# Kernel optimization log

Measured on AMD Instinct MI355X. Metric: run time of the kernel, lower is better.

## Reference

```python
import jax, jax.numpy as jnp
import numpy as np

TEMPERATURE = 0.5


def _cos_sim_flat(a, b):
    # row-normalize then full similarity matrix, flattened (matches torch.mm(a_n, b_n.T).flatten())
    a_n = a / jnp.linalg.norm(a, axis=1, keepdims=True)
    b_n = b / jnp.linalg.norm(b, axis=1, keepdims=True)
    return (a_n @ b_n.T).reshape(-1)


def setup_inputs() -> dict:
    key = jax.random.key(0)
    k1, k2, k3 = jax.random.split(key, 3)
    N, D = 4096, 2048
    return {
        "x_source": jax.random.normal(k1, (N, D), dtype=jnp.float32),
        "x_bc_target": jax.random.normal(k2, (N, D), dtype=jnp.float32),
        "x_raw_target": jax.random.normal(k3, (N, D), dtype=jnp.float32),
    }


def reference(x_source, x_bc_target, x_raw_target):
    sim_pos = _cos_sim_flat(x_source, x_bc_target)  # [N*N]
    sim_neg = _cos_sim_flat(x_source, x_raw_target)  # [N*N]
    # denom = sum_j exp(sim_neg_j / T); loss_i = -log(exp(sim_pos_i/T)/denom)
    # = -sim_pos_i/T + logsumexp(sim_neg/T); mean over i. Same math as the
    # original scalar loops, computed as one fused reduction.
    log_denom = jax.nn.logsumexp(sim_neg / TEMPERATURE)
    cl_loss = jnp.mean(log_denom - sim_pos / TEMPERATURE)
    return cl_loss
```

## Files before the change

### kernel.cpp

```cpp
#include <hip/hip_runtime.h>
#include <hip/hip_bf16.h>

#define NR 4096
#define DD 2048
#define INV_T 2.0f
#define QSCALE 32.0f
#define ACC_TO_LOGIT (INV_T / (QSCALE * QSCALE))
#define QS4 64.0f
#define ACC4_TO_LOGIT (INV_T / (QS4 * QS4))

typedef __attribute__((ext_vector_type(2))) float floatx2;
typedef __attribute__((ext_vector_type(4))) float floatx4;
typedef __attribute__((ext_vector_type(4))) int int4v;
typedef __attribute__((ext_vector_type(8))) int int8v;

static __device__ __forceinline__ void async_copy16(const void* g, void* lds) {
  __builtin_amdgcn_global_load_lds((const __attribute__((address_space(1))) void*)g,
                                   (__attribute__((address_space(3))) void*)lds,
                                   16, 0, 0);
}

static __device__ __forceinline__ unsigned int enc4(float x) {
  float u = fminf(fabsf(x), 6.0f);
  int c = (u >= 0.25f) + (u >= 0.75f) + (u >= 1.25f) + (u >= 1.75f) +
          (u >= 2.5f) + (u >= 3.5f) + (u >= 5.0f);
  return (unsigned)(c | (x < 0.f ? 8 : 0));
}

static __device__ __forceinline__ unsigned int pack8_fp4(
    const float4& v0, const float4& v1, float s) {
  return enc4(v0.x * s)        | (enc4(v0.y * s) << 4)  |
         (enc4(v0.z * s) << 8) | (enc4(v0.w * s) << 12) |
         (enc4(v1.x * s) << 16)| (enc4(v1.y * s) << 20) |
         (enc4(v1.z * s) << 24)| (enc4(v1.w * s) << 28);
}

__global__ __launch_bounds__(256) void normalize_kernel(
    const float* __restrict__ src, const float* __restrict__ bc,
    const float* __restrict__ raw,
    unsigned char* __restrict__ a8row, unsigned int* __restrict__ a4,
    unsigned char* __restrict__ b8, unsigned int* __restrict__ c4,
    float* __restrict__ zbuf) {
  const int row = blockIdx.x;
  const int mat = blockIdx.y;
  const int tid = threadIdx.x;
  const float* base = (mat == 0) ? src : ((mat == 1) ? bc : raw);
  const float4* b4 = (const float4*)(base + (size_t)row * DD);

  if (mat == 1 && row < 17) {
    const int idx = row * 256 + tid;
    if (idx < 2 * DD + 1) zbuf[idx] = 0.f;
  }

  float4 v0 = b4[tid * 2];
  float4 v1 = b4[tid * 2 + 1];
  float ss = v0.x * v0.x + v0.y * v0.y + v0.z * v0.z + v0.w * v0.w +
             v1.x * v1.x + v1.y * v1.y + v1.z * v1.z + v1.w * v1.w;
  #pragma unroll
  for (int off = 32; off > 0; off >>= 1) ss += __shfl_down(ss, off, 64);

  __shared__ float sred[4];
  __shared__ float sinv;
  if ((tid & 63) == 0) sred[tid >> 6] = ss;
  __syncthreads();
  if (tid == 0) sinv = rsqrtf(sred[0] + sred[1] + sred[2] + sred[3]);
  __syncthreads();

  if (mat == 2) {
    c4[row * (DD / 8) + tid] = pack8_fp4(v0, v1, sinv * QS4);
    return;
  }

  const float s = sinv * QSCALE;
  int d0 = __builtin_amdgcn_cvt_pk_fp8_f32(v0.x * s, v0.y * s, 0, false);
  d0 = __builtin_amdgcn_cvt_pk_fp8_f32(v0.z * s, v0.w * s, d0, true);
  int d1 = __builtin_amdgcn_cvt_pk_fp8_f32(v1.x * s, v1.y * s, 0, false);
  d1 = __builtin_amdgcn_cvt_pk_fp8_f32(v1.z * s, v1.w * s, d1, true);
  int2 o; o.x = d0; o.y = d1;
  if (mat == 0) {
    *(int2*)(a8row + (size_t)row * DD + tid * 8) = o;
    a4[row * (DD / 8) + tid] = pack8_fp4(v0, v1, sinv * QS4);
  } else {
    *(int2*)(b8 + (size_t)row * DD + tid * 8) = o;
  }
}

__global__ __launch_bounds__(256, 2) void gemm_expsum_kernel(
    const unsigned char* __restrict__ a4, const unsigned char* __restrict__ c4,
    float* __restrict__ S_part) {
  __shared__ unsigned char As[2][128 * 128];
  __shared__ unsigned char Cs[2][128 * 128];
  const int tid = threadIdx.x;
  const int lane = tid & 63;
  const int wave = tid >> 6;
  const int wr = wave >> 1;
  const int wc = wave & 1;
  const int quad = lane >> 4;
  const int l16 = lane & 15;
  const int bc = blockIdx.x, br = blockIdx.y;

  floatx4 acc[4][4] = {};

  const int wrow = lane >> 3;
  const int csrc = (lane & 7) ^ (wrow & 7);
  const unsigned char* gA[4];
  const unsigned char* gC[4];
  int ldsOff[4];
  #pragma unroll
  for (int q = 0; q < 4; q++) {
    const int m = wave * 4 + q;
    const int row = m * 8 + wrow;
    gA[q] = a4 + (size_t)(br * 128 + row) * 1024 + csrc * 16;
    gC[q] = c4 + (size_t)(bc * 128 + row) * 1024 + csrc * 16;
    ldsOff[q] = m * 1024;
  }

  #pragma unroll
  for (int q = 0; q < 4; q++) {
    async_copy16(gA[q], &As[0][ldsOff[q]]);
    async_copy16(gC[q], &Cs[0][ldsOff[q]]);
    gA[q] += 128; gC[q] += 128;
  }

  const int NKT = DD / 256;
  #pragma unroll 2
  for (int kt = 0; kt < NKT; kt++) {
    const int cur = kt & 1;
    __syncthreads();

    if (kt < NKT - 1) {
      #pragma unroll
      for (int q = 0; q < 4; q++) {
        async_copy16(gA[q], &As[cur ^ 1][ldsOff[q]]);
        async_copy16(gC[q], &Cs[cur ^ 1][ldsOff[q]]);
        gA[q] += 128; gC[q] += 128;
      }
    }

    int4v af[2][4], bf[2][4];
    #pragma unroll
    for (int s = 0; s < 2; s++) {
      #pragma unroll
      for (int i = 0; i < 4; i++) {
        const int r = wr * 64 + i * 16 + l16;
        const int pc = (s * 4 + quad) ^ (r & 7);
        af[s][i] = *(const int4v*)&As[cur][r * 128 + pc * 16];
      }
      #pragma unroll
      for (int j = 0; j < 4; j++) {
        const int r = wc * 64 + j * 16 + l16;
        const int pc = (s * 4 + quad) ^ (r & 7);
        bf[s][j] = *(const int4v*)&Cs[cur][r * 128 + pc * 16];
      }
    }
    #pragma unroll
    for (int s = 0; s < 2; s++)
      #pragma unroll
      for (int i = 0; i < 4; i++) {
        const int8v a8v = int8v{af[s][i][0], af[s][i][1], af[s][i][2],
                                af[s][i][3], 0, 0, 0, 0};
        #pragma unroll
        for (int j = 0; j < 4; j++) {
          const int8v b8v = int8v{bf[s][j][0], bf[s][j][1], bf[s][j][2],
                                  bf[s][j][3], 0, 0, 0, 0};
          acc[i][j] = __builtin_amdgcn_mfma_scale_f32_16x16x128_f8f6f4(
              a8v, b8v, acc[i][j], 4 , 4 ,
              0, 0x7F7F7F7F, 0, 0x7F7F7F7F );
        }
      }
  }

  float local = 0.f;
  #pragma unroll
  for (int i = 0; i < 4; i++)
    #pragma unroll
    for (int j = 0; j < 4; j++)
      #pragma unroll
      for (int r = 0; r < 4; r++)
        local += __expf(acc[i][j][r] * ACC4_TO_LOGIT);
  #pragma unroll
  for (int off = 32; off > 0; off >>= 1) local += __shfl_down(local, off, 64);
  __shared__ float red[4];
  if (lane == 0) red[wave] = local;
  __syncthreads();
  if (tid == 0) S_part[br * 32 + bc] = red[0] + red[1] + red[2] + red[3];
}

__global__ __launch_bounds__(256) void colsum_finalize_kernel(
    const unsigned char* __restrict__ a8, const unsigned char* __restrict__ b8,
    float* __restrict__ s_a, float* __restrict__ s_b,
    float* __restrict__ counter, const float* __restrict__ S_part,
    float* __restrict__ out) {
  __shared__ float lds[32 * 264];
  const int tid = threadIdx.x;
  const int rt = tid >> 3;
  const int ct = tid & 7;
  const int cg = blockIdx.x & 7;
  const int rg = blockIdx.x >> 3;
  const int cbase = cg * 256 + ct * 32;
  const int rbase = rg * 256 + rt;

  float accA[32], accB[32];
  #pragma unroll
  for (int i = 0; i < 32; i++) { accA[i] = 0.f; accB[i] = 0.f; }

  #pragma unroll
  for (int k = 0; k < 8; k++) {
    const size_t off = (size_t)(rbase + k * 32) * DD + cbase;
    const int8v ra = *(const int8v*)(a8 + off);
    const int8v rb = *(const int8v*)(b8 + off);
    #pragma unroll
    for (int u = 0; u < 8; u++) {
      floatx2 lo = __builtin_amdgcn_cvt_pk_f32_fp8(ra[u], false);
      floatx2 hi = __builtin_amdgcn_cvt_pk_f32_fp8(ra[u], true);
      accA[u * 4 + 0] += lo[0]; accA[u * 4 + 1] += lo[1];
      accA[u * 4 + 2] += hi[0]; accA[u * 4 + 3] += hi[1];
      lo = __builtin_amdgcn_cvt_pk_f32_fp8(rb[u], false);
      hi = __builtin_amdgcn_cvt_pk_f32_fp8(rb[u], true);
      accB[u * 4 + 0] += lo[0]; accB[u * 4 + 1] += lo[1];
      accB[u * 4 + 2] += hi[0]; accB[u * 4 + 3] += hi[1];
    }
  }

  #pragma unroll
  for (int i = 0; i < 32; i += 4)
    *(floatx4*)&lds[rt * 264 + ct * 32 + i] =
        floatx4{accA[i], accA[i + 1], accA[i + 2], accA[i + 3]};
  __syncthreads();
  float sA = 0.f;
  #pragma unroll 8
  for (int r = 0; r < 32; r++) sA += lds[r * 264 + tid];
  atomicAdd(&s_a[cg * 256 + tid], sA);
  __syncthreads();

  #pragma unroll
  for (int i = 0; i < 32; i += 4)
    *(floatx4*)&lds[rt * 264 + ct * 32 + i] =
        floatx4{accB[i], accB[i + 1], accB[i + 2], accB[i + 3]};
  __syncthreads();
  float sB = 0.f;
  #pragma unroll 8
  for (int r = 0; r < 32; r++) sB += lds[r * 264 + tid];
  atomicAdd(&s_b[cg * 256 + tid], sB);

  __threadfence();
  __syncthreads();
  __shared__ bool amLast;
  if (tid == 0) amLast = (atomicAdd(counter, 1.0f) == 127.0f);
  __syncthreads();
  if (!amLast) return;
  __threadfence();

  float dot = 0.f;
  for (int d = tid; d < DD; d += 256)
    dot += atomicAdd(&s_a[d], 0.f) * atomicAdd(&s_b[d], 0.f);
  float se = 0.f;
  for (int i = tid; i < 1024; i += 256) se += S_part[i];

  #pragma unroll
  for (int off = 32; off > 0; off >>= 1) {
    dot += __shfl_down(dot, off, 64);
    se += __shfl_down(se, off, 64);
  }
  __shared__ float redd[4], reds[4];
  if ((tid & 63) == 0) { redd[tid >> 6] = dot; reds[tid >> 6] = se; }
  __syncthreads();
  if (tid == 0) {
    const float dt = redd[0] + redd[1] + redd[2] + redd[3];
    const float st = reds[0] + reds[1] + reds[2] + reds[3];
    out[0] = logf(st) - dt * (ACC_TO_LOGIT / ((float)NR * (float)NR));
  }
}

extern "C" void kernel_launch(void* const* d_in, const int* in_sizes, int n_in,
                              void* d_out, int out_size, void* d_ws, size_t ws_size,
                              hipStream_t stream) {
  const float* src = (const float*)d_in[0];
  const float* bc  = (const float*)d_in[1];
  const float* raw = (const float*)d_in[2];

  char* ws = (char*)d_ws;
  unsigned char* a8row = (unsigned char*)ws;
  unsigned char* b8 = (unsigned char*)(ws + (size_t)8 * 1024 * 1024);
  unsigned int* a4  = (unsigned int*)(ws + (size_t)16 * 1024 * 1024);
  unsigned int* c4  = (unsigned int*)(ws + (size_t)20 * 1024 * 1024);
  float* zbuf  = (float*)(ws + (size_t)24 * 1024 * 1024);
  float* s_a   = zbuf;
  float* s_b   = zbuf + DD;
  float* counter = zbuf + 2 * DD;
  float* S_part = (float*)(ws + (size_t)24 * 1024 * 1024 + 20480);

  normalize_kernel<<<dim3(NR, 3), 256, 0, stream>>>(src, bc, raw, a8row, a4,
                                                    b8, c4, zbuf);
  gemm_expsum_kernel<<<dim3(32, 32), 256, 0, stream>>>(
      (const unsigned char*)a4, (const unsigned char*)c4, S_part);
  colsum_finalize_kernel<<<128, 256, 0, stream>>>(a8row, b8, s_a, s_b, counter,
                                                  S_part, (float*)d_out);
}
```

Before: 163.9 us.

## Fuse column sums into normalization, drop fp8 copies, remap GEMM tiles per XCD

The normalize kernel now handles 16 rows per block and accumulates the normalized column sums of source and positive-target in fp32 registers. It then reduces them through LDS and adds them atomically into global buffers. This removes the fp8 intermediate matrices and the separate column-sum pass that re-read them. The GEMM block index is remapped so neighbouring tiles land on the same XCD for better L2 reuse. A small zero kernel and a single-block finalize kernel replace the last-block counter logic, which adds launches but makes the positive-term sum more precise.

```diff
diff --git a/kernel.cpp b/kernel.cpp
--- a/kernel.cpp
+++ b/kernel.cpp
@@ -1,11 +1,8 @@
 #include <hip/hip_runtime.h>
-#include <hip/hip_bf16.h>
 
 #define NR 4096
 #define DD 2048
 #define INV_T 2.0f
-#define QSCALE 32.0f
-#define ACC_TO_LOGIT (INV_T / (QSCALE * QSCALE))
 #define QS4 64.0f
 #define ACC4_TO_LOGIT (INV_T / (QS4 * QS4))
 
@@ -35,53 +32,77 @@
          (enc4(v1.z * s) << 24)| (enc4(v1.w * s) << 28);
 }
 
-__global__ __launch_bounds__(256) void normalize_kernel(
+__global__ __launch_bounds__(256) void zero_kernel(floatx4* z) {
+  #pragma unroll
+  for (int i = 0; i < 4; i++)
+    z[threadIdx.x + 256 * i] = floatx4{0.f, 0.f, 0.f, 0.f};
+}
+
+__global__ __launch_bounds__(256) void normalize_colsum_kernel(
     const float* __restrict__ src, const float* __restrict__ bc,
     const float* __restrict__ raw,
-    unsigned char* __restrict__ a8row, unsigned int* __restrict__ a4,
-    unsigned char* __restrict__ b8, unsigned int* __restrict__ c4,
-    float* __restrict__ zbuf) {
-  const int row = blockIdx.x;
+    unsigned int* __restrict__ a4, unsigned int* __restrict__ c4,
+    float* __restrict__ s_a, float* __restrict__ s_b) {
   const int mat = blockIdx.y;
   const int tid = threadIdx.x;
+  const int lane = tid & 63;
+  const int wave = tid >> 6;
   const float* base = (mat == 0) ? src : ((mat == 1) ? bc : raw);
-  const float4* b4 = (const float4*)(base + (size_t)row * DD);
-
-  if (mat == 1 && row < 17) {
-    const int idx = row * 256 + tid;
-    if (idx < 2 * DD + 1) zbuf[idx] = 0.f;
-  }
-
-  float4 v0 = b4[tid * 2];
-  float4 v1 = b4[tid * 2 + 1];
-  float ss = v0.x * v0.x + v0.y * v0.y + v0.z * v0.z + v0.w * v0.w +
-             v1.x * v1.x + v1.y * v1.y + v1.z * v1.z + v1.w * v1.w;
-  #pragma unroll
-  for (int off = 32; off > 0; off >>= 1) ss += __shfl_down(ss, off, 64);
-
-  __shared__ float sred[4];
-  __shared__ float sinv;
-  if ((tid & 63) == 0) sred[tid >> 6] = ss;
+  unsigned int* q4 = (mat == 0) ? a4 : c4;
+
+  float acc[32];
+  #pragma unroll
+  for (int i = 0; i < 32; i++) acc[i] = 0.f;
+
+  #pragma unroll
+  for (int r = 0; r < 4; r++) {
+    const int row = blockIdx.x * 16 + wave * 4 + r;
+    const float4* rp = (const float4*)(base + (size_t)row * DD);
+    float4 v[8];
+    #pragma unroll
+    for (int c = 0; c < 4; c++) {
+      v[2 * c]     = rp[lane * 2 + 128 * c];
+      v[2 * c + 1] = rp[lane * 2 + 1 + 128 * c];
+    }
+    float ss = 0.f;
+    #pragma unroll
+    for (int c = 0; c < 8; c++)
+      ss += v[c].x * v[c].x + v[c].y * v[c].y + v[c].z * v[c].z + v[c].w * v[c].w;
+    #pragma unroll
+    for (int off = 1; off < 64; off <<= 1) ss += __shfl_xor(ss, off, 64);
+    const float sinv = rsqrtf(ss);
+
+    if (mat != 2) {
+      #pragma unroll
+      for (int c = 0; c < 8; c++) {
+        acc[c * 4 + 0] += v[c].x * sinv; acc[c * 4 + 1] += v[c].y * sinv;
+        acc[c * 4 + 2] += v[c].z * sinv; acc[c * 4 + 3] += v[c].w * sinv;
+      }
+    }
+    if (mat != 1) {
+      const float s4 = sinv * QS4;
+      #pragma unroll
+      for (int c = 0; c < 4; c++)
+        q4[row * 256 + lane + 64 * c] = pack8_fp4(v[2 * c], v[2 * c + 1], s4);
+    }
+  }
+  if (mat == 2) return;
+
+  __shared__ float lsum[4][2048];
+  #pragma unroll
+  for (int c = 0; c < 4; c++) {
+    *(floatx4*)&lsum[wave][8 * lane + 512 * c] =
+        floatx4{acc[8 * c], acc[8 * c + 1], acc[8 * c + 2], acc[8 * c + 3]};
+    *(floatx4*)&lsum[wave][8 * lane + 512 * c + 4] =
+        floatx4{acc[8 * c + 4], acc[8 * c + 5], acc[8 * c + 6], acc[8 * c + 7]};
+  }
   __syncthreads();
-  if (tid == 0) sinv = rsqrtf(sred[0] + sred[1] + sred[2] + sred[3]);
-  __syncthreads();
-
-  if (mat == 2) {
-    c4[row * (DD / 8) + tid] = pack8_fp4(v0, v1, sinv * QS4);
-    return;
-  }
-
-  const float s = sinv * QSCALE;
-  int d0 = __builtin_amdgcn_cvt_pk_fp8_f32(v0.x * s, v0.y * s, 0, false);
-  d0 = __builtin_amdgcn_cvt_pk_fp8_f32(v0.z * s, v0.w * s, d0, true);
-  int d1 = __builtin_amdgcn_cvt_pk_fp8_f32(v1.x * s, v1.y * s, 0, false);
-  d1 = __builtin_amdgcn_cvt_pk_fp8_f32(v1.z * s, v1.w * s, d1, true);
-  int2 o; o.x = d0; o.y = d1;
-  if (mat == 0) {
-    *(int2*)(a8row + (size_t)row * DD + tid * 8) = o;
-    a4[row * (DD / 8) + tid] = pack8_fp4(v0, v1, sinv * QS4);
-  } else {
-    *(int2*)(b8 + (size_t)row * DD + tid * 8) = o;
+  float* dst = (mat == 0) ? s_a : s_b;
+  #pragma unroll
+  for (int k = 0; k < 8; k++) {
+    const int col = tid + 256 * k;
+    atomicAdd(&dst[col],
+              lsum[0][col] + lsum[1][col] + lsum[2][col] + lsum[3][col]);
   }
 }
 
@@ -97,7 +118,12 @@
   const int wc = wave & 1;
   const int quad = lane >> 4;
   const int l16 = lane & 15;
-  const int bc = blockIdx.x, br = blockIdx.y;
+
+  const int lin = blockIdx.y * 32 + blockIdx.x;
+  const int xcd = lin & 7;
+  const int idx = lin >> 3;
+  const int br = (xcd >> 1) * 8 + (idx >> 4);
+  const int bc = (xcd & 1) * 16 + (idx & 15);
 
   floatx4 acc[4][4] = {};
 
@@ -186,81 +212,20 @@
   if (tid == 0) S_part[br * 32 + bc] = red[0] + red[1] + red[2] + red[3];
 }
 
-__global__ __launch_bounds__(256) void colsum_finalize_kernel(
-    const unsigned char* __restrict__ a8, const unsigned char* __restrict__ b8,
-    float* __restrict__ s_a, float* __restrict__ s_b,
-    float* __restrict__ counter, const float* __restrict__ S_part,
-    float* __restrict__ out) {
-  __shared__ float lds[32 * 264];
+__global__ __launch_bounds__(256) void finalize_kernel(
+    const float* __restrict__ s_a, const float* __restrict__ s_b,
+    const float* __restrict__ S_part, float* __restrict__ out) {
   const int tid = threadIdx.x;
-  const int rt = tid >> 3;
-  const int ct = tid & 7;
-  const int cg = blockIdx.x & 7;
-  const int rg = blockIdx.x >> 3;
-  const int cbase = cg * 256 + ct * 32;
-  const int rbase = rg * 256 + rt;
-
-  float accA[32], accB[32];
-  #pragma unroll
-  for (int i = 0; i < 32; i++) { accA[i] = 0.f; accB[i] = 0.f; }
-
-  #pragma unroll
-  for (int k = 0; k < 8; k++) {
-    const size_t off = (size_t)(rbase + k * 32) * DD + cbase;
-    const int8v ra = *(const int8v*)(a8 + off);
-    const int8v rb = *(const int8v*)(b8 + off);
-    #pragma unroll
-    for (int u = 0; u < 8; u++) {
-      floatx2 lo = __builtin_amdgcn_cvt_pk_f32_fp8(ra[u], false);
-      floatx2 hi = __builtin_amdgcn_cvt_pk_f32_fp8(ra[u], true);
-      accA[u * 4 + 0] += lo[0]; accA[u * 4 + 1] += lo[1];
-      accA[u * 4 + 2] += hi[0]; accA[u * 4 + 3] += hi[1];
-      lo = __builtin_amdgcn_cvt_pk_f32_fp8(rb[u], false);
-      hi = __builtin_amdgcn_cvt_pk_f32_fp8(rb[u], true);
-      accB[u * 4 + 0] += lo[0]; accB[u * 4 + 1] += lo[1];
-      accB[u * 4 + 2] += hi[0]; accB[u * 4 + 3] += hi[1];
-    }
-  }
-
-  #pragma unroll
-  for (int i = 0; i < 32; i += 4)
-    *(floatx4*)&lds[rt * 264 + ct * 32 + i] =
-        floatx4{accA[i], accA[i + 1], accA[i + 2], accA[i + 3]};
-  __syncthreads();
-  float sA = 0.f;
-  #pragma unroll 8
-  for (int r = 0; r < 32; r++) sA += lds[r * 264 + tid];
-  atomicAdd(&s_a[cg * 256 + tid], sA);
-  __syncthreads();
-
-  #pragma unroll
-  for (int i = 0; i < 32; i += 4)
-    *(floatx4*)&lds[rt * 264 + ct * 32 + i] =
-        floatx4{accB[i], accB[i + 1], accB[i + 2], accB[i + 3]};
-  __syncthreads();
-  float sB = 0.f;
-  #pragma unroll 8
-  for (int r = 0; r < 32; r++) sB += lds[r * 264 + tid];
-  atomicAdd(&s_b[cg * 256 + tid], sB);
-
-  __threadfence();
-  __syncthreads();
-  __shared__ bool amLast;
-  if (tid == 0) amLast = (atomicAdd(counter, 1.0f) == 127.0f);
-  __syncthreads();
-  if (!amLast) return;
-  __threadfence();
-
-  float dot = 0.f;
-  for (int d = tid; d < DD; d += 256)
-    dot += atomicAdd(&s_a[d], 0.f) * atomicAdd(&s_b[d], 0.f);
-  float se = 0.f;
-  for (int i = tid; i < 1024; i += 256) se += S_part[i];
-
+  float dot = 0.f, se = 0.f;
+  #pragma unroll
+  for (int k = 0; k < 8; k++)
+    dot += s_a[tid + 256 * k] * s_b[tid + 256 * k];
+  #pragma unroll
+  for (int k = 0; k < 4; k++) se += S_part[tid + 256 * k];
   #pragma unroll
   for (int off = 32; off > 0; off >>= 1) {
     dot += __shfl_down(dot, off, 64);
-    se += __shfl_down(se, off, 64);
+    se  += __shfl_down(se, off, 64);
   }
   __shared__ float redd[4], reds[4];
   if ((tid & 63) == 0) { redd[tid >> 6] = dot; reds[tid >> 6] = se; }
@@ -268,7 +233,7 @@
   if (tid == 0) {
     const float dt = redd[0] + redd[1] + redd[2] + redd[3];
     const float st = reds[0] + reds[1] + reds[2] + reds[3];
-    out[0] = logf(st) - dt * (ACC_TO_LOGIT / ((float)NR * (float)NR));
+    out[0] = logf(st) - dt * (INV_T / ((float)NR * (float)NR));
   }
 }
 
@@ -280,20 +245,17 @@
   const float* raw = (const float*)d_in[2];
 
   char* ws = (char*)d_ws;
-  unsigned char* a8row = (unsigned char*)ws;
-  unsigned char* b8 = (unsigned char*)(ws + (size_t)8 * 1024 * 1024);
-  unsigned int* a4  = (unsigned int*)(ws + (size_t)16 * 1024 * 1024);
-  unsigned int* c4  = (unsigned int*)(ws + (size_t)20 * 1024 * 1024);
-  float* zbuf  = (float*)(ws + (size_t)24 * 1024 * 1024);
-  float* s_a   = zbuf;
-  float* s_b   = zbuf + DD;
-  float* counter = zbuf + 2 * DD;
-  float* S_part = (float*)(ws + (size_t)24 * 1024 * 1024 + 20480);
-
-  normalize_kernel<<<dim3(NR, 3), 256, 0, stream>>>(src, bc, raw, a8row, a4,
-                                                    b8, c4, zbuf);
+  unsigned int* a4 = (unsigned int*)ws;
+  unsigned int* c4 = (unsigned int*)(ws + (size_t)4 * 1024 * 1024);
+  float* zb  = (float*)(ws + (size_t)8 * 1024 * 1024);
+  float* s_a = zb;
+  float* s_b = zb + DD;
+  float* S_part = (float*)(ws + (size_t)8 * 1024 * 1024 + 32 * 1024);
+
+  zero_kernel<<<1, 256, 0, stream>>>((floatx4*)zb);
+  normalize_colsum_kernel<<<dim3(NR / 16, 3), 256, 0, stream>>>(
+      src, bc, raw, a4, c4, s_a, s_b);
   gemm_expsum_kernel<<<dim3(32, 32), 256, 0, stream>>>(
       (const unsigned char*)a4, (const unsigned char*)c4, S_part);
-  colsum_finalize_kernel<<<128, 256, 0, stream>>>(a8row, b8, s_a, s_b, counter,
-                                                  S_part, (float*)d_out);
-}
+  finalize_kernel<<<1, 256, 0, stream>>>(s_a, s_b, S_part, (float*)d_out);
+}
```

Result: faster. 149.4 us (-8.9%).
